# Optimization experiments

Measured on AMD Instinct MI355X. Metric: run time of the kernel, lower is better.

## Reference

```python
import jax, jax.numpy as jnp
import numpy as np

NUM_HEADS = 8
D_MODEL = 512
D_Q = D_MODEL // NUM_HEADS
B, S = 4, 2048


def setup_inputs() -> dict:
    key = jax.random.key(0)
    ks = jax.random.split(key, 7)
    bound = 1.0 / np.sqrt(D_MODEL)  # kaiming_uniform with a=sqrt(5) on fan_in=d_model
    return {
        "x_query": jax.random.normal(ks[0], (B, S, D_MODEL), dtype=jnp.float32),
        "x_key": jax.random.normal(ks[1], (B, S, D_MODEL), dtype=jnp.float32),
        "x_value": jax.random.normal(ks[2], (B, S, D_MODEL), dtype=jnp.float32),
        "Q": jax.random.uniform(ks[3], (NUM_HEADS, D_MODEL, D_Q), minval=-bound, maxval=bound, dtype=jnp.float32),
        "K": jax.random.uniform(ks[4], (NUM_HEADS, D_MODEL, D_Q), minval=-bound, maxval=bound, dtype=jnp.float32),
        "V": jax.random.uniform(ks[5], (NUM_HEADS, D_MODEL, D_Q), minval=-bound, maxval=bound, dtype=jnp.float32),
        "Wout": jax.random.uniform(ks[6], (D_MODEL, D_MODEL), minval=-bound, maxval=bound, dtype=jnp.float32),
    }


def reference(x_query, x_key, x_value, Q, K, V, Wout):
    # per-head projections: [B,S,d_model] x [H,d_model,d_q] -> [B,H,S,d_q]
    q = jnp.einsum('bsd,hdq->bhsq', x_query, Q)
    k = jnp.einsum('bsd,hdq->bhsq', x_key, K)
    v = jnp.einsum('bsd,hdq->bhsq', x_value, V)
    scale = 1.0 / jnp.sqrt(jnp.asarray(q.shape[-1], q.dtype))
    scores = jnp.einsum('bhsq,bhtq->bhst', q, k) * scale  # [B,H,S,S]
    attn = jax.nn.softmax(scores, axis=-1)
    heads = jnp.einsum('bhst,bhtq->bhsq', attn, v)  # [B,H,S,d_q]
    # faithful to original: .view(B, S, -1) on [B,H,S,d_q] layout (no transpose)
    concat = heads.reshape(heads.shape[0], heads.shape[2], -1)
    return concat @ Wout.T
```

## Files before the change

### kernel.cpp

```cpp
#include <hip/hip_runtime.h>
#include <math.h>

#define BATCH 4
#define SEQ   2048
#define DM    512
#define NH    8
#define DQ    64
#define BS    (BATCH*SEQ)
#define APAD  72

#define QSCALE 0.18033688011112042f

typedef short  short8   __attribute__((ext_vector_type(8)));
typedef float  floatx4  __attribute__((ext_vector_type(4)));
typedef float  floatx16 __attribute__((ext_vector_type(16)));
typedef unsigned short ushort8 __attribute__((ext_vector_type(8)));
typedef unsigned uintx2 __attribute__((ext_vector_type(2)));
typedef unsigned uintx4 __attribute__((ext_vector_type(4)));

__device__ __forceinline__ unsigned short f2bf(float f) {
    return (unsigned short)((__float_as_uint(f) + 0x8000u) >> 16);
}
__device__ __forceinline__ unsigned pack2bf(float a, float b) {
    unsigned ua = __float_as_uint(a) + 0x8000u;
    unsigned ub = __float_as_uint(b) + 0x8000u;
    return __builtin_amdgcn_perm(ub, ua, 0x07060302u);
}
__device__ __forceinline__ unsigned cvtpk(float a, float b) {
    unsigned r;
    asm("v_cvt_pk_bf16_f32 %0, %1, %2" : "=v"(r) : "v"(a), "v"(b));
    return r;
}

__global__ __launch_bounds__(256) void convert_w_kernel(
    const float* __restrict__ Wq, const float* __restrict__ Wk,
    const float* __restrict__ Wv, const float* __restrict__ Wo,
    unsigned short* __restrict__ wt, unsigned short* __restrict__ wo)
{
    const int which = blockIdx.y;
    const int idx = blockIdx.x * 256 + threadIdx.x;
    if (which == 3) {
        float4 v = *(const float4*)(Wo + (size_t)idx * 4);
        uint2 o;
        o.x = pack2bf(v.x, v.y);
        o.y = pack2bf(v.z, v.w);
        *(uint2*)(wo + (size_t)idx * 4) = o;
    } else {
        const float* W = (which == 0) ? Wq : (which == 1) ? Wk : Wv;
        const int n   = idx & 511;
        const int dd0 = (idx >> 9) * 4;
        const int h = n >> 6, d = n & 63;
        uint2 o;
        o.x = pack2bf(W[((size_t)h * DM + dd0 + 0) * DQ + d],
                      W[((size_t)h * DM + dd0 + 1) * DQ + d]);
        o.y = pack2bf(W[((size_t)h * DM + dd0 + 2) * DQ + d],
                      W[((size_t)h * DM + dd0 + 3) * DQ + d]);
        *(uint2*)(wt + (size_t)which * (DM * DM) + (size_t)n * DM + dd0) = o;
    }
}

__global__ __launch_bounds__(256) void qkv_gemm_kernel(
    const float* __restrict__ Xq, const float* __restrict__ Xk,
    const float* __restrict__ Xv, const unsigned short* __restrict__ wt,
    unsigned short* __restrict__ Oq, unsigned short* __restrict__ Ok,
    unsigned short* __restrict__ Ovt)
{
    __shared__ unsigned short As[64][APAD];
    __shared__ unsigned short Bs[128][APAD];

    const int which = blockIdx.z;
    const float* X = (which == 0) ? Xq : (which == 1) ? Xk : Xv;
    const unsigned short* Bt = wt + (size_t)which * (DM * DM);

    const int m0 = blockIdx.x * 64;
    const int n0 = blockIdx.y * 128;
    const int t = threadIdx.x, w = t >> 6, lane = t & 63;
    const int quad = lane >> 4, qr = lane & 15;
    const int arow = t >> 4;
    const int acol = (t & 15) * 4;
    const int brow = t >> 3;
    const int bcol = (t & 7) * 8;
    const int mw = 32 * (w >> 1), nw = 64 * (w & 1);

    floatx4 acc[2][4] = {};
    float4  areg[4];
    ushort8 breg[4];

    #pragma unroll
    for (int i = 0; i < 4; ++i)
        areg[i] = *(const float4*)(X + (size_t)(m0 + i * 16 + arow) * DM + acol);
    #pragma unroll
    for (int i = 0; i < 4; ++i)
        breg[i] = *(const ushort8*)(Bt + (size_t)(n0 + i * 32 + brow) * DM + bcol);

    for (int k0 = 0; k0 < DM; k0 += 64) {
        __syncthreads();
        #pragma unroll
        for (int i = 0; i < 4; ++i) {
            uint2 o;
            o.x = pack2bf(areg[i].x, areg[i].y);
            o.y = pack2bf(areg[i].z, areg[i].w);
            *(uint2*)&As[i * 16 + arow][acol] = o;
        }
        #pragma unroll
        for (int i = 0; i < 4; ++i)
            *(ushort8*)&Bs[i * 32 + brow][bcol] = breg[i];
        __syncthreads();

        if (k0 + 64 < DM) {
            #pragma unroll
            for (int i = 0; i < 4; ++i)
                areg[i] = *(const float4*)(X + (size_t)(m0 + i * 16 + arow) * DM + k0 + 64 + acol);
            #pragma unroll
            for (int i = 0; i < 4; ++i)
                breg[i] = *(const ushort8*)(Bt + (size_t)(n0 + i * 32 + brow) * DM + k0 + 64 + bcol);
        }

        #pragma unroll
        for (int kh = 0; kh < 2; ++kh) {
            short8 af[2], bf[4];
            #pragma unroll
            for (int si = 0; si < 2; ++si)
                af[si] = *(const short8*)&As[mw + 16 * si + qr][kh * 32 + quad * 8];
            #pragma unroll
            for (int sj = 0; sj < 4; ++sj)
                bf[sj] = *(const short8*)&Bs[nw + 16 * sj + qr][kh * 32 + quad * 8];
            #pragma unroll
            for (int si = 0; si < 2; ++si)
                #pragma unroll
                for (int sj = 0; sj < 4; ++sj)
                    acc[si][sj] = __builtin_amdgcn_mfma_f32_16x16x32_bf16(
                        af[si], bf[sj], acc[si][sj], 0, 0, 0);
        }
    }

    if (which == 0) {
        #pragma unroll
        for (int si = 0; si < 2; ++si) {
            #pragma unroll
            for (int sj = 0; sj < 4; ++sj) {
                const int col = n0 + nw + 16 * sj + qr;
                const int h = col >> 6, d = col & 63;
                #pragma unroll
                for (int r = 0; r < 4; ++r) {
                    const int row = m0 + mw + 16 * si + quad * 4 + r;
                    const int b = row >> 11, s = row & (SEQ - 1);
                    Oq[((size_t)(b * NH + h) * SEQ + s) * DQ + d] = f2bf(acc[si][sj][r] * QSCALE);
                }
            }
        }
    } else if (which == 1) {
        #pragma unroll
        for (int si = 0; si < 2; ++si) {
            #pragma unroll
            for (int sj = 0; sj < 4; ++sj) {
                const int col = n0 + nw + 16 * sj + qr;
                const int h = col >> 6, d = col & 63;
                #pragma unroll
                for (int r = 0; r < 4; ++r) {
                    const int row = m0 + mw + 16 * si + quad * 4 + r;
                    const int b = row >> 11, s = row & (SEQ - 1);
                    Ok[(size_t)(b * NH + h) * (SEQ * DQ)
                       + (size_t)(((s >> 5) * 4 + (d >> 4)) << 9)
                       + ((((d >> 3) & 1) << 5) + (s & 31)) * 8 + (d & 7)] = f2bf(acc[si][sj][r]);
                }
            }
        }
    } else {
        #pragma unroll
        for (int si = 0; si < 2; ++si) {
            #pragma unroll
            for (int sj = 0; sj < 4; ++sj) {
                const int col = n0 + nw + 16 * sj + qr;
                const int h = col >> 6, d = col & 63;
                #pragma unroll
                for (int r = 0; r < 4; ++r) {
                    const int row = m0 + mw + 16 * si + quad * 4 + r;
                    const int b = row >> 11, s = row & (SEQ - 1);
                    Ovt[(size_t)(b * NH + h) * (SEQ * DQ)
                        + (size_t)((s >> 6) << 12) + (((s >> 5) & 1) << 11)
                        + ((d >> 5) << 10) + (((s >> 4) & 1) << 9)
                        + ((((s >> 3) & 1) << 5) + (d & 31)) * 8 + (s & 7)] = f2bf(acc[si][sj][r]);
                }
            }
        }
    }
}

__global__ __launch_bounds__(256) void out_gemm_kernel(
    const unsigned short* __restrict__ A, const unsigned short* __restrict__ Bt,
    float* __restrict__ C)
{
    __shared__ unsigned short As[64][APAD];
    __shared__ unsigned short Bs[64][APAD];

    const int m0 = blockIdx.x * 64;
    const int n0 = blockIdx.y * 64;
    const int t = threadIdx.x, w = t >> 6, lane = t & 63;
    const int quad = lane >> 4, qr = lane & 15;
    const int brow = t >> 3;
    const int bcol = (t & 7) * 8;
    const int mw = 32 * (w >> 1), nw = 32 * (w & 1);

    floatx4 acc[2][2] = {};
    ushort8 areg[2], breg[2];

    #pragma unroll
    for (int i = 0; i < 2; ++i) {
        areg[i] = *(const ushort8*)(A + (size_t)(m0 + i * 32 + brow) * DM + bcol);
        breg[i] = *(const ushort8*)(Bt + (size_t)(n0 + i * 32 + brow) * DM + bcol);
    }

    for (int k0 = 0; k0 < DM; k0 += 64) {
        __syncthreads();
        #pragma unroll
        for (int i = 0; i < 2; ++i) {
            *(ushort8*)&As[i * 32 + brow][bcol] = areg[i];
            *(ushort8*)&Bs[i * 32 + brow][bcol] = breg[i];
        }
        __syncthreads();

        if (k0 + 64 < DM) {
            #pragma unroll
            for (int i = 0; i < 2; ++i) {
                areg[i] = *(const ushort8*)(A + (size_t)(m0 + i * 32 + brow) * DM + k0 + 64 + bcol);
                breg[i] = *(const ushort8*)(Bt + (size_t)(n0 + i * 32 + brow) * DM + k0 + 64 + bcol);
            }
        }

        #pragma unroll
        for (int kh = 0; kh < 2; ++kh) {
            short8 af[2], bf[2];
            #pragma unroll
            for (int si = 0; si < 2; ++si)
                af[si] = *(const short8*)&As[mw + 16 * si + qr][kh * 32 + quad * 8];
            #pragma unroll
            for (int sj = 0; sj < 2; ++sj)
                bf[sj] = *(const short8*)&Bs[nw + 16 * sj + qr][kh * 32 + quad * 8];
            #pragma unroll
            for (int si = 0; si < 2; ++si)
                #pragma unroll
                for (int sj = 0; sj < 2; ++sj)
                    acc[si][sj] = __builtin_amdgcn_mfma_f32_16x16x32_bf16(
                        af[si], bf[sj], acc[si][sj], 0, 0, 0);
        }
    }

    #pragma unroll
    for (int si = 0; si < 2; ++si) {
        #pragma unroll
        for (int sj = 0; sj < 2; ++sj) {
            const int col = n0 + nw + 16 * sj + qr;
            #pragma unroll
            for (int r = 0; r < 4; ++r) {
                const int row = m0 + mw + 16 * si + quad * 4 + r;
                C[(size_t)row * DM + col] = acc[si][sj][r];
            }
        }
    }
}

__global__ __launch_bounds__(512, 2) void attn_kernel(
    const unsigned short* __restrict__ Qp, const unsigned short* __restrict__ Kf,
    const unsigned short* __restrict__ Vf, unsigned short* __restrict__ Hd)
{
    __shared__ float epi[128 * 66 + 128];

    const int f    = blockIdx.x;
    const int xcd  = f & 7;
    const int slot = f >> 3;
    const int tile = slot & 15;
    const int bhi  = (slot >> 4) * 8 + xcd;
    const int b = bhi >> 3, h = bhi & 7;

    const int s0 = tile * 128;
    const size_t bh   = (size_t)(b * NH + h);
    const size_t base = bh * SEQ * DQ;

    const int t    = threadIdx.x;
    const int w    = t >> 6;
    const int lane = t & 63;
    const int qh   = w >> 1;
    const int kh   = w & 1;
    const int ln31 = lane & 31;
    const int lh   = lane >> 5;

    short8 bq[4];
    {
        const unsigned short* gq = Qp + base + (size_t)(s0 + 32 * qh + ln31) * DQ + lh * 8;
        #pragma unroll
        for (int s = 0; s < 4; ++s)
            bq[s] = *(const short8*)(gq + 16 * s);
    }

    short8 vones;
    #pragma unroll
    for (int i = 0; i < 8; ++i) vones[i] = (short)0x3F80;

    const unsigned short* pK = Kf + base + ((size_t)kh << 11) + (size_t)lane * 8;
    const unsigned short* pV = Vf + base + ((size_t)kh << 11) + (size_t)lane * 8;

    floatx16 accO[2] = {};
    floatx16 accL   = {};

    short8 ak[4], bv[4];
    #pragma unroll
    for (int s = 0; s < 4; ++s)
        ak[s] = *(const short8*)(pK + s * 512);
    #pragma unroll
    for (int a = 0; a < 2; ++a)
        #pragma unroll
        for (int s = 0; s < 2; ++s)
            bv[a * 2 + s] = *(const short8*)(pV + a * 1024 + s * 512);

    for (int kt = 0; kt < SEQ; kt += 64) {
        floatx16 z = {};
        __builtin_amdgcn_s_setprio(1);
        #pragma unroll
        for (int s = 0; s < 4; ++s)
            z = __builtin_amdgcn_mfma_f32_32x32x16_bf16(ak[s], bq[s], z, 0, 0, 0);
        __builtin_amdgcn_s_setprio(0);

        const int ktn = (kt + 64 < SEQ) ? kt + 64 : kt;
        {
            const unsigned short* nK = pK + ((size_t)(ktn >> 5) << 11);
            #pragma unroll
            for (int s = 0; s < 4; ++s)
                ak[s] = *(const short8*)(nK + s * 512);
        }

        unsigned wg[4][2];
        #pragma unroll
        for (int g = 0; g < 4; ++g) {
            const float p0 = __builtin_amdgcn_exp2f(z[4 * g + 0]);
            const float p1 = __builtin_amdgcn_exp2f(z[4 * g + 1]);
            const float p2 = __builtin_amdgcn_exp2f(z[4 * g + 2]);
            const float p3 = __builtin_amdgcn_exp2f(z[4 * g + 3]);
            wg[g][0] = cvtpk(p0, p1);
            wg[g][1] = cvtpk(p2, p3);
        }

        const uintx2 e0 = __builtin_amdgcn_permlane32_swap(wg[0][0], wg[1][0], false, false);
        const uintx2 e1 = __builtin_amdgcn_permlane32_swap(wg[0][1], wg[1][1], false, false);
        const uintx2 e2 = __builtin_amdgcn_permlane32_swap(wg[2][0], wg[3][0], false, false);
        const uintx2 e3 = __builtin_amdgcn_permlane32_swap(wg[2][1], wg[3][1], false, false);
        uintx4 ua0, ua1;
        ua0[0] = e0[0]; ua0[1] = e1[0]; ua0[2] = e0[1]; ua0[3] = e1[1];
        ua1[0] = e2[0]; ua1[1] = e3[0]; ua1[2] = e2[1]; ua1[3] = e3[1];
        const short8 ap0 = __builtin_bit_cast(short8, ua0);
        const short8 ap1 = __builtin_bit_cast(short8, ua1);

        __builtin_amdgcn_s_setprio(1);
        #pragma unroll
        for (int a = 0; a < 2; ++a) {
            accO[a] = __builtin_amdgcn_mfma_f32_32x32x16_bf16(ap0, bv[a * 2 + 0], accO[a], 0, 0, 0);
            accO[a] = __builtin_amdgcn_mfma_f32_32x32x16_bf16(ap1, bv[a * 2 + 1], accO[a], 0, 0, 0);
        }
        accL = __builtin_amdgcn_mfma_f32_32x32x16_bf16(ap0, vones, accL, 0, 0, 0);
        accL = __builtin_amdgcn_mfma_f32_32x32x16_bf16(ap1, vones, accL, 0, 0, 0);
        __builtin_amdgcn_s_setprio(0);

        {
            const unsigned short* nV = pV + ((size_t)(ktn >> 6) << 12);
            #pragma unroll
            for (int a = 0; a < 2; ++a)
                #pragma unroll
                for (int s = 0; s < 2; ++s)
                    bv[a * 2 + s] = *(const short8*)(nV + a * 1024 + s * 512);
        }
    }

    float* Obuf = epi;
    float* lbuf = epi + 128 * 66;

    if (kh == 0) {
        if (ln31 == 0) {
            #pragma unroll
            for (int r = 0; r < 16; ++r) {
                const int qrow = (r & 3) + 8 * (r >> 2) + 4 * lh;
                lbuf[32 * qh + qrow] = accL[r];
            }
        }
        #pragma unroll
        for (int a = 0; a < 2; ++a)
            #pragma unroll
            for (int r = 0; r < 16; ++r) {
                const int qrow = (r & 3) + 8 * (r >> 2) + 4 * lh;
                Obuf[(32 * qh + qrow) * 66 + 32 * a + ln31] = accO[a][r];
            }
    }
    __syncthreads();

    if (kh == 1) {
        float inv[16];
        #pragma unroll
        for (int r = 0; r < 16; ++r) {
            const int qrow = (r & 3) + 8 * (r >> 2) + 4 * lh;
            inv[r] = 1.0f / (accL[r] + lbuf[32 * qh + qrow]);
        }
        #pragma unroll
        for (int a = 0; a < 2; ++a)
            #pragma unroll
            for (int r = 0; r < 16; ++r) {
                const int qrow = (r & 3) + 8 * (r >> 2) + 4 * lh;
                const float o = accO[a][r] + Obuf[(32 * qh + qrow) * 66 + 32 * a + ln31];
                Hd[base + (size_t)(s0 + 32 * qh + qrow) * DQ + 32 * a + ln31] = f2bf(o * inv[r]);
            }
    }
}

extern "C" void kernel_launch(void* const* d_in, const int* in_sizes, int n_in,
                              void* d_out, int out_size, void* d_ws, size_t ws_size,
                              hipStream_t stream) {
    const float* xq = (const float*)d_in[0];
    const float* xk = (const float*)d_in[1];
    const float* xv = (const float*)d_in[2];
    const float* Qw = (const float*)d_in[3];
    const float* Kw = (const float*)d_in[4];
    const float* Vw = (const float*)d_in[5];
    const float* Wo = (const float*)d_in[6];
    float* out = (float*)d_out;

    unsigned short* ws = (unsigned short*)d_ws;
    unsigned short* wt    = ws;
    unsigned short* wo    = ws + (size_t)786432;
    unsigned short* q_ws  = ws + (size_t)1048576;
    unsigned short* k_ws  = ws + (size_t)5242880;
    unsigned short* vt_ws = ws + (size_t)9437184;
    unsigned short* h_ws  = ws + (size_t)13631488;

    convert_w_kernel<<<dim3(256, 4), 256, 0, stream>>>(Qw, Kw, Vw, Wo, wt, wo);
    qkv_gemm_kernel<<<dim3(128, 4, 3), 256, 0, stream>>>(xq, xk, xv, wt, q_ws, k_ws, vt_ws);
    attn_kernel<<<dim3(512), 512, 0, stream>>>(q_ws, k_ws, vt_ws, h_ws);
    out_gemm_kernel<<<dim3(128, 8), 256, 0, stream>>>(h_ws, wo, out);
}
```

Baseline: 180.5 us.

## Pre-convert X to bf16 and stage GEMM tiles via direct global-to-LDS loads

```diff
diff --git a/kernel.cpp b/kernel.cpp
--- a/kernel.cpp
+++ b/kernel.cpp
@@ -7,7 +7,6 @@
 #define NH    8
 #define DQ    64
 #define BS    (BATCH*SEQ)
-#define APAD  72
 
 #define QSCALE 0.18033688011112042f
 
@@ -30,6 +29,11 @@
     unsigned r;
     asm("v_cvt_pk_bf16_f32 %0, %1, %2" : "=v"(r) : "v"(a), "v"(b));
     return r;
+}
+__device__ __forceinline__ void gload16(const unsigned short* g, unsigned short* l) {
+    __builtin_amdgcn_global_load_lds(
+        (const __attribute__((address_space(1))) unsigned int*)g,
+        (__attribute__((address_space(3))) unsigned int*)l, 16, 0, 0);
 }
 
 __global__ __launch_bounds__(256) void convert_w_kernel(
@@ -59,74 +63,66 @@
     }
 }
 
+__global__ __launch_bounds__(256) void x_convert_kernel(
+    const float* __restrict__ Xq, const float* __restrict__ Xk,
+    const float* __restrict__ Xv, unsigned short* __restrict__ xb)
+{
+    const int which = blockIdx.y;
+    const float* X = (which == 0) ? Xq : (which == 1) ? Xk : Xv;
+    const size_t i = ((size_t)blockIdx.x * 256 + threadIdx.x) * 8;
+    const float4 a = *(const float4*)(X + i);
+    const float4 b = *(const float4*)(X + i + 4);
+    uint4 o;
+    o.x = pack2bf(a.x, a.y); o.y = pack2bf(a.z, a.w);
+    o.z = pack2bf(b.x, b.y); o.w = pack2bf(b.z, b.w);
+    *(uint4*)(xb + (size_t)which * ((size_t)BS * DM) + i) = o;
+}
+
 __global__ __launch_bounds__(256) void qkv_gemm_kernel(
-    const float* __restrict__ Xq, const float* __restrict__ Xk,
-    const float* __restrict__ Xv, const unsigned short* __restrict__ wt,
+    const unsigned short* __restrict__ xb, const unsigned short* __restrict__ wt,
     unsigned short* __restrict__ Oq, unsigned short* __restrict__ Ok,
     unsigned short* __restrict__ Ovt)
 {
-    __shared__ unsigned short As[64][APAD];
-    __shared__ unsigned short Bs[128][APAD];
+    __shared__ unsigned short As[128][64];
+    __shared__ unsigned short Bs[128][64];
 
     const int which = blockIdx.z;
-    const float* X = (which == 0) ? Xq : (which == 1) ? Xk : Xv;
+    const unsigned short* A  = xb + (size_t)which * ((size_t)BS * DM);
     const unsigned short* Bt = wt + (size_t)which * (DM * DM);
 
-    const int m0 = blockIdx.x * 64;
+    const int m0 = blockIdx.x * 128;
     const int n0 = blockIdx.y * 128;
     const int t = threadIdx.x, w = t >> 6, lane = t & 63;
     const int quad = lane >> 4, qr = lane & 15;
-    const int arow = t >> 4;
-    const int acol = (t & 15) * 4;
-    const int brow = t >> 3;
-    const int bcol = (t & 7) * 8;
-    const int mw = 32 * (w >> 1), nw = 64 * (w & 1);
-
-    floatx4 acc[2][4] = {};
-    float4  areg[4];
-    ushort8 breg[4];
-
-    #pragma unroll
-    for (int i = 0; i < 4; ++i)
-        areg[i] = *(const float4*)(X + (size_t)(m0 + i * 16 + arow) * DM + acol);
-    #pragma unroll
-    for (int i = 0; i < 4; ++i)
-        breg[i] = *(const ushort8*)(Bt + (size_t)(n0 + i * 32 + brow) * DM + bcol);
+    const int mw = 64 * (w >> 1), nw = 64 * (w & 1);
+
+    const int lr = lane >> 3;
+    const int swoff = (((lane & 7) ^ lr) * 8) + lr * DM;
+
+    floatx4 acc[4][4] = {};
 
     for (int k0 = 0; k0 < DM; k0 += 64) {
+        if (k0) __syncthreads();
+        #pragma unroll
+        for (int c = 0; c < 4; ++c) {
+            const int rb = 8 * (w + 4 * c);
+            gload16(A  + (size_t)(m0 + rb) * DM + k0 + swoff, &As[rb][0]);
+            gload16(Bt + (size_t)(n0 + rb) * DM + k0 + swoff, &Bs[rb][0]);
+        }
         __syncthreads();
-        #pragma unroll
-        for (int i = 0; i < 4; ++i) {
-            uint2 o;
-            o.x = pack2bf(areg[i].x, areg[i].y);
-            o.y = pack2bf(areg[i].z, areg[i].w);
-            *(uint2*)&As[i * 16 + arow][acol] = o;
-        }
-        #pragma unroll
-        for (int i = 0; i < 4; ++i)
-            *(ushort8*)&Bs[i * 32 + brow][bcol] = breg[i];
-        __syncthreads();
-
-        if (k0 + 64 < DM) {
-            #pragma unroll
-            for (int i = 0; i < 4; ++i)
-                areg[i] = *(const float4*)(X + (size_t)(m0 + i * 16 + arow) * DM + k0 + 64 + acol);
-            #pragma unroll
-            for (int i = 0; i < 4; ++i)
-                breg[i] = *(const ushort8*)(Bt + (size_t)(n0 + i * 32 + brow) * DM + k0 + 64 + bcol);
-        }
 
         #pragma unroll
         for (int kh = 0; kh < 2; ++kh) {
-            short8 af[2], bf[4];
-            #pragma unroll
-            for (int si = 0; si < 2; ++si)
-                af[si] = *(const short8*)&As[mw + 16 * si + qr][kh * 32 + quad * 8];
+            const int cs = (kh * 32 + quad * 8) ^ ((qr & 7) * 8);
+            short8 af[4], bf[4];
+            #pragma unroll
+            for (int si = 0; si < 4; ++si)
+                af[si] = *(const short8*)&As[mw + 16 * si + qr][cs];
             #pragma unroll
             for (int sj = 0; sj < 4; ++sj)
-                bf[sj] = *(const short8*)&Bs[nw + 16 * sj + qr][kh * 32 + quad * 8];
-            #pragma unroll
-            for (int si = 0; si < 2; ++si)
+                bf[sj] = *(const short8*)&Bs[nw + 16 * sj + qr][cs];
+            #pragma unroll
+            for (int si = 0; si < 4; ++si)
                 #pragma unroll
                 for (int sj = 0; sj < 4; ++sj)
                     acc[si][sj] = __builtin_amdgcn_mfma_f32_16x16x32_bf16(
@@ -136,7 +132,7 @@
 
     if (which == 0) {
         #pragma unroll
-        for (int si = 0; si < 2; ++si) {
+        for (int si = 0; si < 4; ++si) {
             #pragma unroll
             for (int sj = 0; sj < 4; ++sj) {
                 const int col = n0 + nw + 16 * sj + qr;
@@ -151,7 +147,7 @@
         }
     } else if (which == 1) {
         #pragma unroll
-        for (int si = 0; si < 2; ++si) {
+        for (int si = 0; si < 4; ++si) {
             #pragma unroll
             for (int sj = 0; sj < 4; ++sj) {
                 const int col = n0 + nw + 16 * sj + qr;
@@ -168,7 +164,7 @@
         }
     } else {
         #pragma unroll
-        for (int si = 0; si < 2; ++si) {
+        for (int si = 0; si < 4; ++si) {
             #pragma unroll
             for (int sj = 0; sj < 4; ++sj) {
                 const int col = n0 + nw + 16 * sj + qr;
@@ -191,56 +187,48 @@
     const unsigned short* __restrict__ A, const unsigned short* __restrict__ Bt,
     float* __restrict__ C)
 {
-    __shared__ unsigned short As[64][APAD];
-    __shared__ unsigned short Bs[64][APAD];
+    __shared__ unsigned short As[64][64];
+    __shared__ unsigned short Bs[128][64];
 
     const int m0 = blockIdx.x * 64;
-    const int n0 = blockIdx.y * 64;
+    const int n0 = blockIdx.y * 128;
     const int t = threadIdx.x, w = t >> 6, lane = t & 63;
     const int quad = lane >> 4, qr = lane & 15;
-    const int brow = t >> 3;
-    const int bcol = (t & 7) * 8;
-    const int mw = 32 * (w >> 1), nw = 32 * (w & 1);
-
-    floatx4 acc[2][2] = {};
-    ushort8 areg[2], breg[2];
-
-    #pragma unroll
-    for (int i = 0; i < 2; ++i) {
-        areg[i] = *(const ushort8*)(A + (size_t)(m0 + i * 32 + brow) * DM + bcol);
-        breg[i] = *(const ushort8*)(Bt + (size_t)(n0 + i * 32 + brow) * DM + bcol);
-    }
+    const int mw = 32 * (w >> 1), nw = 64 * (w & 1);
+
+    const int lr = lane >> 3;
+    const int swoff = (((lane & 7) ^ lr) * 8) + lr * DM;
+
+    floatx4 acc[2][4] = {};
 
     for (int k0 = 0; k0 < DM; k0 += 64) {
+        if (k0) __syncthreads();
+        #pragma unroll
+        for (int c = 0; c < 2; ++c) {
+            const int rb = 8 * (w + 4 * c);
+            gload16(A + (size_t)(m0 + rb) * DM + k0 + swoff, &As[rb][0]);
+        }
+        #pragma unroll
+        for (int c = 0; c < 4; ++c) {
+            const int rb = 8 * (w + 4 * c);
+            gload16(Bt + (size_t)(n0 + rb) * DM + k0 + swoff, &Bs[rb][0]);
+        }
         __syncthreads();
-        #pragma unroll
-        for (int i = 0; i < 2; ++i) {
-            *(ushort8*)&As[i * 32 + brow][bcol] = areg[i];
-            *(ushort8*)&Bs[i * 32 + brow][bcol] = breg[i];
-        }
-        __syncthreads();
-
-        if (k0 + 64 < DM) {
-            #pragma unroll
-            for (int i = 0; i < 2; ++i) {
-                areg[i] = *(const ushort8*)(A + (size_t)(m0 + i * 32 + brow) * DM + k0 + 64 + bcol);
-                breg[i] = *(const ushort8*)(Bt + (size_t)(n0 + i * 32 + brow) * DM + k0 + 64 + bcol);
-            }
-        }
 
         #pragma unroll
         for (int kh = 0; kh < 2; ++kh) {
-            short8 af[2], bf[2];
+            const int cs = (kh * 32 + quad * 8) ^ ((qr & 7) * 8);
+            short8 af[2], bf[4];
             #pragma unroll
             for (int si = 0; si < 2; ++si)
-                af[si] = *(const short8*)&As[mw + 16 * si + qr][kh * 32 + quad * 8];
-            #pragma unroll
-            for (int sj = 0; sj < 2; ++sj)
-                bf[sj] = *(const short8*)&Bs[nw + 16 * sj + qr][kh * 32 + quad * 8];
+                af[si] = *(const short8*)&As[mw + 16 * si + qr][cs];
+            #pragma unroll
+            for (int sj = 0; sj < 4; ++sj)
+                bf[sj] = *(const short8*)&Bs[nw + 16 * sj + qr][cs];
             #pragma unroll
             for (int si = 0; si < 2; ++si)
                 #pragma unroll
-                for (int sj = 0; sj < 2; ++sj)
+                for (int sj = 0; sj < 4; ++sj)
                     acc[si][sj] = __builtin_amdgcn_mfma_f32_16x16x32_bf16(
                         af[si], bf[sj], acc[si][sj], 0, 0, 0);
         }
@@ -249,7 +237,7 @@
     #pragma unroll
     for (int si = 0; si < 2; ++si) {
         #pragma unroll
-        for (int sj = 0; sj < 2; ++sj) {
+        for (int sj = 0; sj < 4; ++sj) {
             const int col = n0 + nw + 16 * sj + qr;
             #pragma unroll
             for (int r = 0; r < 4; ++r) {
@@ -427,10 +415,12 @@
     unsigned short* q_ws  = ws + (size_t)1048576;
     unsigned short* k_ws  = ws + (size_t)5242880;
     unsigned short* vt_ws = ws + (size_t)9437184;
+    unsigned short* xb    = ws + (size_t)13631488;
     unsigned short* h_ws  = ws + (size_t)13631488;
 
     convert_w_kernel<<<dim3(256, 4), 256, 0, stream>>>(Qw, Kw, Vw, Wo, wt, wo);
-    qkv_gemm_kernel<<<dim3(128, 4, 3), 256, 0, stream>>>(xq, xk, xv, wt, q_ws, k_ws, vt_ws);
+    x_convert_kernel<<<dim3(2048, 3), 256, 0, stream>>>(xq, xk, xv, xb);
+    qkv_gemm_kernel<<<dim3(64, 4, 3), 256, 0, stream>>>(xb, wt, q_ws, k_ws, vt_ws);
     attn_kernel<<<dim3(512), 512, 0, stream>>>(q_ws, k_ws, vt_ws, h_ws);
-    out_gemm_kernel<<<dim3(128, 8), 256, 0, stream>>>(h_ws, wo, out);
-}
+    out_gemm_kernel<<<dim3(128, 4), 256, 0, stream>>>(h_ws, wo, out);
+}
```

Result: no change. 181.6 us (+0.6%).
